# Optimization experiments

Hardware: AMD Instinct MI355X
Metric: run time of the kernel (lower is better)

The kernel has to match this reference:

```python
import jax, jax.numpy as jnp
import numpy as np

N = 100000      # num nodes
E = 3200000     # num edges (avg degree 32)
F_IN = 512      # num_features
HID = 16        # hidden dim hard-coded in GCN.__init__
C = 40          # num_classes


def setup_inputs() -> dict:
    key = jax.random.key(0)
    k = jax.random.split(key, 6)
    x = jax.random.normal(k[0], (N, F_IN), dtype=jnp.float32)
    edge_index = jax.random.randint(k[1], (2, E), 0, N)
    edge_weight = jax.random.uniform(k[2], (E,), dtype=jnp.float32)
    W1 = jax.random.normal(k[3], (F_IN, HID), dtype=jnp.float32) / np.sqrt(F_IN).astype(np.float32)
    b1 = jnp.zeros((HID,), jnp.float32)
    W2 = jax.random.normal(k[4], (HID, C), dtype=jnp.float32) / np.sqrt(HID).astype(np.float32)
    b2 = jnp.zeros((C,), jnp.float32)
    return {"x": x, "edge_weight": edge_weight, "W1": W1, "b1": b1,
            "W2": W2, "b2": b2, "edge_index": edge_index}


def _gcn_norm(edge_index, edge_weight, n):
    # PyG gcn_norm with add_self_loops=True, fill_value=1.0
    row = jnp.concatenate([edge_index[0], jnp.arange(n)])
    col = jnp.concatenate([edge_index[1], jnp.arange(n)])
    w = jnp.concatenate([edge_weight, jnp.ones((n,), edge_weight.dtype)])
    deg = jax.ops.segment_sum(w, col, num_segments=n)
    dinv = jnp.where(deg > 0, jax.lax.rsqrt(deg), 0.0)
    norm = dinv[row] * w * dinv[col]
    return row, col, norm


def _gcn_conv(x, W, b, row, col, norm, n):
    h = x @ W                                   # [N, out] linear first (out dim small)
    msg = h[row] * norm[:, None]                # gather + scale  [E+N, out]
    out = jax.ops.segment_sum(msg, col, num_segments=n)  # scatter-add
    return out + b


def reference(x, edge_weight, W1, b1, W2, b2, edge_index):
    n = x.shape[0]
    row, col, norm = _gcn_norm(edge_index, edge_weight, n)  # cached=True: shared by both layers
    h = jax.nn.relu(_gcn_conv(x, W1, b1, row, col, norm, n))
    # F.dropout(training=self.training) is identity in eval mode
    h = _gcn_conv(h, W2, b2, row, col, norm, n)
    return jax.nn.log_softmax(h, axis=1)
```

## Files before the change

kernel.cpp:

```cpp
#include <hip/hip_runtime.h>
#include <hip/hip_bf16.h>

#define HID 16
#define CLS 40
#define FIN 512
#define TILE 4000
#define NBP 512

typedef unsigned int uint;
typedef unsigned short ushort;

__device__ __forceinline__ ushort f2bf(float f) {
    uint u = __float_as_uint(f);
    u += 0x7FFF + ((u >> 16) & 1);
    return (ushort)(u >> 16);
}
__device__ __forceinline__ float bflo(uint u) { return __uint_as_float(u << 16); }
__device__ __forceinline__ float bfhi(uint u) { return __uint_as_float(u & 0xFFFF0000u); }
__device__ __forceinline__ float wdec(uint a) {
    return __uint_as_float((a >> 17) << 16);
}

__global__ __launch_bounds__(256) void scan1_k(const int* __restrict__ cnt,
                                               int* __restrict__ bsum, int M) {
    __shared__ int ws[4];
    int b = blockIdx.x, t = threadIdx.x;
    int i0 = b * 1024 + t * 4;
    int s = 0;
#pragma unroll
    for (int q = 0; q < 4; ++q) if (i0 + q < M) s += cnt[i0 + q];
    for (int d = 32; d > 0; d >>= 1) s += __shfl_xor(s, d);
    int lane = t & 63, wid = t >> 6;
    if (lane == 0) ws[wid] = s;
    __syncthreads();
    if (t == 0) bsum[b] = ws[0] + ws[1] + ws[2] + ws[3];
}

__global__ __launch_bounds__(256) void scan3_k(const int* __restrict__ cnt,
                                               const int* __restrict__ bsumRaw,
                                               int* __restrict__ sout, int M, int G) {
    __shared__ int sb[1024];
    __shared__ int wsumA[4], wbaseA[4];
    __shared__ int wsumB[4], wbaseB[4];
    int t = threadIdx.x;
    int lane = t & 63, wid = t >> 6;
    {
        int i0 = t * 4;
        int c[4];
#pragma unroll
        for (int q = 0; q < 4; ++q) c[q] = (i0 + q < G) ? bsumRaw[i0 + q] : 0;
        int s = c[0] + c[1] + c[2] + c[3];
        int v = s;
        for (int d = 1; d < 64; d <<= 1) { int u = __shfl_up(v, d); if (lane >= d) v += u; }
        if (lane == 63) wsumA[wid] = v;
        __syncthreads();
        if (t == 0) { int r = 0; for (int q = 0; q < 4; ++q) { wbaseA[q] = r; r += wsumA[q]; } }
        __syncthreads();
        int o = v - s + wbaseA[wid];
#pragma unroll
        for (int q = 0; q < 4; ++q) { sb[i0 + q] = o; o += c[q]; }
    }
    __syncthreads();
    {
        int b = blockIdx.x;
        int i0 = b * 1024 + t * 4;
        int c[4];
#pragma unroll
        for (int q = 0; q < 4; ++q) c[q] = (i0 + q < M) ? cnt[i0 + q] : 0;
        int s = c[0] + c[1] + c[2] + c[3];
        int v = s;
        for (int d = 1; d < 64; d <<= 1) { int u = __shfl_up(v, d); if (lane >= d) v += u; }
        if (lane == 63) wsumB[wid] = v;
        __syncthreads();
        if (t == 0) { int r = 0; for (int q = 0; q < 4; ++q) { wbaseB[q] = r; r += wsumB[q]; } }
        __syncthreads();
        int o = v - s + wbaseB[wid] + sb[b];
#pragma unroll
        for (int q = 0; q < 4; ++q) {
            if (i0 + q < M) { sout[i0 + q] = o; o += c[q]; }
        }
    }
}

__global__ __launch_bounds__(256) void bk_count_k(const int* __restrict__ col,
                                                  int* __restrict__ bcnt,
                                                  int E, int NB, int ABLK) {
    __shared__ int hist[NBP];
    int t = threadIdx.x, blk = blockIdx.x;
    for (int i = t; i < NBP; i += 256) hist[i] = 0;
    __syncthreads();
    int e0 = blk * TILE, e1 = min(E, e0 + TILE);
    for (int e = e0 + t; e < e1; e += 256) atomicAdd(&hist[col[e] >> 8], 1);
    __syncthreads();
    for (int b = t; b < NB; b += 256) bcnt[b * ABLK + blk] = hist[b];
}

__global__ __launch_bounds__(256) void bk_scatter_k(const int* __restrict__ row,
                                                    const int* __restrict__ col,
                                                    const float* __restrict__ w,
                                                    const int* __restrict__ sbcnt,
                                                    int2* __restrict__ bpack,
                                                    int E, int NB, int ABLK) {
    __shared__ int2 stage[TILE];
    __shared__ ushort stageB[TILE];
    __shared__ int hist[NBP], cur[NBP], gbase[NBP];
    __shared__ int wsum[4], wbase[4];
    int t = threadIdx.x, blk = blockIdx.x;
    for (int i = t; i < NBP; i += 256) hist[i] = 0;
    __syncthreads();
    int e0 = blk * TILE, e1 = min(E, e0 + TILE);
    for (int e = e0 + t; e < e1; e += 256) atomicAdd(&hist[col[e] >> 8], 1);
    __syncthreads();
    {
        int c0 = hist[2 * t], c1 = hist[2 * t + 1];
        int s = c0 + c1;
        int lane = t & 63, wid = t >> 6;
        int v = s;
        for (int d = 1; d < 64; d <<= 1) { int u = __shfl_up(v, d); if (lane >= d) v += u; }
        if (lane == 63) wsum[wid] = v;
        __syncthreads();
        if (t == 0) { int r = 0; for (int q = 0; q < 4; ++q) { wbase[q] = r; r += wsum[q]; } }
        __syncthreads();
        int excl = v - s + wbase[wid];
        int s0 = 2 * t, s1 = 2 * t + 1;
        cur[s0] = excl;
        gbase[s0] = ((s0 < NB) ? sbcnt[s0 * ABLK + blk] : 0) - excl;
        cur[s1] = excl + c0;
        gbase[s1] = ((s1 < NB) ? sbcnt[s1 * ABLK + blk] : 0) - (excl + c0);
    }
    __syncthreads();
    for (int e = e0 + t; e < e1; e += 256) {
        int c = col[e];
        int bkt = c >> 8, cl = c & 255;
        int lr = atomicAdd(&cur[bkt], 1);
        stage[lr] = make_int2(row[e] | (cl << 17), __float_as_int(w[e]));
        stageB[lr] = (ushort)bkt;
    }
    __syncthreads();
    int cntE = e1 - e0;
    for (int s = t; s < cntE; s += 256) {
        int bkt = stageB[s];
        bpack[gbase[bkt] + s] = stage[s];
    }
}

__global__ __launch_bounds__(512) void seg_build_k(const int2* __restrict__ bpack,
                                                   const int* __restrict__ sbcnt,
                                                   int* __restrict__ off,
                                                   float* __restrict__ dinv,
                                                   uint* __restrict__ fin,
                                                   int E, int NB, int ABLK, int NN) {
    __shared__ int cntL[256];
    __shared__ float degL[256];
    __shared__ int curL[256];
    __shared__ int wtot[8];
    int t = threadIdx.x, b = blockIdx.x;
    if (t < 256) { cntL[t] = 0; degL[t] = 0.f; }
    __syncthreads();
    int p0 = sbcnt[b * ABLK];
    int p1 = (b + 1 < NB) ? sbcnt[(b + 1) * ABLK] : E;
    for (int p = p0 + t; p < p1; p += 512) {
        int2 pk = bpack[p];
        int cl = (pk.x >> 17) & 255;
        atomicAdd(&cntL[cl], 1);
        atomicAdd(&degL[cl], __int_as_float(pk.y));
    }
    __syncthreads();
    int c = (t < 256) ? cntL[t] : 0;
    int lane = t & 63, wid = t >> 6;
    int v = c;
    for (int d = 1; d < 64; d <<= 1) { int u = __shfl_up(v, d); if (lane >= d) v += u; }
    if (lane == 63) wtot[wid] = v;
    __syncthreads();
    if (t < 256) {
        int base = p0;
        for (int q = 0; q < wid; ++q) base += wtot[q];
        int excl = base + v - c;
        int node = b * 256 + t;
        off[node] = excl;
        curL[t] = excl;
        dinv[node] = rsqrtf(1.0f + degL[t]);
    }
    if (b == NB - 1 && t == 0) off[NN] = E;
    __syncthreads();
    for (int p = p0 + t; p < p1; p += 512) {
        int2 pk = bpack[p];
        uint src = (uint)pk.x & 0x1FFFFu;
        int cl = (pk.x >> 17) & 255;
        uint u = (uint)pk.y + 0x8000u;
        int pos = atomicAdd(&curL[cl], 1);
        fin[pos] = src | ((u >> 16) << 17);
    }
}

__global__ __launch_bounds__(256) void gemm1_k(const float* __restrict__ x,
                                               const float* __restrict__ W1,
                                               const float* __restrict__ dinv,
                                               uint* __restrict__ g, int n) {
    __shared__ float4 w1s[FIN * HID / 4 + FIN / 4];
    {
        const float4* s4 = (const float4*)W1;
        for (int i = threadIdx.x; i < FIN * HID / 4; i += 256)
            w1s[i + (i >> 4)] = s4[i];
    }
    __syncthreads();
    int r = blockIdx.x * 64 + (threadIdx.x >> 2);
    if (r >= n) return;
    int sub = threadIdx.x & 3;
    const float4* xr = (const float4*)(x + (size_t)r * FIN);
    float acc[HID];
#pragma unroll
    for (int c = 0; c < HID; ++c) acc[c] = 0.f;
    for (int q = 0; q < FIN / 16; ++q) {
        float4 xv = xr[q * 4 + sub];
        int kbase = q * 16 + sub * 4;
        const float4* w4 = &w1s[kbase * 4 + (kbase >> 2)];
#pragma unroll
        for (int e = 0; e < 4; ++e) {
            float xe = (e == 0) ? xv.x : (e == 1) ? xv.y : (e == 2) ? xv.z : xv.w;
#pragma unroll
            for (int j = 0; j < 4; ++j) {
                float4 wv = w4[e * 4 + j];
                acc[4 * j + 0] += xe * wv.x;
                acc[4 * j + 1] += xe * wv.y;
                acc[4 * j + 2] += xe * wv.z;
                acc[4 * j + 3] += xe * wv.w;
            }
        }
    }
#pragma unroll
    for (int c = 0; c < HID; ++c) {
        acc[c] += __shfl_xor(acc[c], 1, 4);
        acc[c] += __shfl_xor(acc[c], 2, 4);
    }
    float f0, f1, f2, f3;
    {
        float t0 = (sub & 2) ? acc[8] : acc[0], t4 = (sub & 2) ? acc[12] : acc[4];
        f0 = (sub & 1) ? t4 : t0;
        float u0 = (sub & 2) ? acc[9] : acc[1], u4 = (sub & 2) ? acc[13] : acc[5];
        f1 = (sub & 1) ? u4 : u0;
        float v0 = (sub & 2) ? acc[10] : acc[2], v4 = (sub & 2) ? acc[14] : acc[6];
        f2 = (sub & 1) ? v4 : v0;
        float w0 = (sub & 2) ? acc[11] : acc[3], w4v = (sub & 2) ? acc[15] : acc[7];
        f3 = (sub & 1) ? w4v : w0;
    }
    float di = dinv[r];
    uint lo = (uint)f2bf(di * f0) | ((uint)f2bf(di * f1) << 16);
    uint hi = (uint)f2bf(di * f2) | ((uint)f2bf(di * f3) << 16);
    ((uint2*)(g + (size_t)r * 8))[sub] = make_uint2(lo, hi);
}

__global__ __launch_bounds__(256) void agg1_k(const uint* __restrict__ g,
                                              const float* __restrict__ dinv,
                                              const int* __restrict__ off,
                                              const uint* __restrict__ fin,
                                              const float* __restrict__ b1,
                                              uint* __restrict__ g1, int n) {
    int tid = blockIdx.x * 256 + threadIdx.x;
    int i = tid >> 3;
    if (i >= n) return;
    int lane = tid & 7;
    uint sv = g[(size_t)i * 8 + lane];
    float lo0 = bflo(sv), hi0 = bfhi(sv);
    float lo1 = 0.f, hi1 = 0.f, lo2 = 0.f, hi2 = 0.f, lo3 = 0.f, hi3 = 0.f;
    int p = off[i], e = off[i + 1];
    for (; p + 3 < e; p += 4) {
        uint a = fin[p], b = fin[p + 1], c = fin[p + 2], d = fin[p + 3];
        uint ga = g[(size_t)(a & 0x1FFFFu) * 8 + lane];
        uint gb = g[(size_t)(b & 0x1FFFFu) * 8 + lane];
        uint gc = g[(size_t)(c & 0x1FFFFu) * 8 + lane];
        uint gd = g[(size_t)(d & 0x1FFFFu) * 8 + lane];
        float wa = wdec(a), wb = wdec(b), wc = wdec(c), wdv = wdec(d);
        lo0 += wa * bflo(ga); hi0 += wa * bfhi(ga);
        lo1 += wb * bflo(gb); hi1 += wb * bfhi(gb);
        lo2 += wc * bflo(gc); hi2 += wc * bfhi(gc);
        lo3 += wdv * bflo(gd); hi3 += wdv * bfhi(gd);
    }
    for (; p < e; ++p) {
        uint a = fin[p];
        uint ga = g[(size_t)(a & 0x1FFFFu) * 8 + lane];
        float wa = wdec(a);
        lo0 += wa * bflo(ga); hi0 += wa * bfhi(ga);
    }
    float di = dinv[i];
    float vlo = fmaxf(di * ((lo0 + lo1) + (lo2 + lo3)) + b1[2 * lane], 0.f);
    float vhi = fmaxf(di * ((hi0 + hi1) + (hi2 + hi3)) + b1[2 * lane + 1], 0.f);
    g1[(size_t)i * 8 + lane] = (uint)f2bf(di * vlo) | ((uint)f2bf(di * vhi) << 16);
}

__global__ __launch_bounds__(256) void agg2out_k(const uint* __restrict__ g1,
                                                 const float* __restrict__ dinv,
                                                 const int* __restrict__ off,
                                                 const uint* __restrict__ fin,
                                                 const float* __restrict__ W2,
                                                 const float* __restrict__ b2,
                                                 float* __restrict__ out, int n) {
    __shared__ float w2s[HID * CLS];
    __shared__ float b2s[CLS];
    for (int q = threadIdx.x; q < HID * CLS; q += 256) w2s[q] = W2[q];
    if (threadIdx.x < CLS) b2s[threadIdx.x] = b2[threadIdx.x];
    __syncthreads();
    int tid = blockIdx.x * 256 + threadIdx.x;
    int i = tid >> 3;
    if (i >= n) return;
    int lane = tid & 7;
    uint sv = g1[(size_t)i * 8 + lane];
    float lo0 = bflo(sv), hi0 = bfhi(sv);
    float lo1 = 0.f, hi1 = 0.f, lo2 = 0.f, hi2 = 0.f, lo3 = 0.f, hi3 = 0.f;
    int p = off[i], e = off[i + 1];
    for (; p + 3 < e; p += 4) {
        uint a = fin[p], b = fin[p + 1], c = fin[p + 2], d = fin[p + 3];
        uint ga = g1[(size_t)(a & 0x1FFFFu) * 8 + lane];
        uint gb = g1[(size_t)(b & 0x1FFFFu) * 8 + lane];
        uint gc = g1[(size_t)(c & 0x1FFFFu) * 8 + lane];
        uint gd = g1[(size_t)(d & 0x1FFFFu) * 8 + lane];
        float wa = wdec(a), wb = wdec(b), wc = wdec(c), wdv = wdec(d);
        lo0 += wa * bflo(ga); hi0 += wa * bfhi(ga);
        lo1 += wb * bflo(gb); hi1 += wb * bfhi(gb);
        lo2 += wc * bflo(gc); hi2 += wc * bfhi(gc);
        lo3 += wdv * bflo(gd); hi3 += wdv * bfhi(gd);
    }
    for (; p < e; ++p) {
        uint a = fin[p];
        uint ga = g1[(size_t)(a & 0x1FFFFu) * 8 + lane];
        float wa = wdec(a);
        lo0 += wa * bflo(ga); hi0 += wa * bfhi(ga);
    }
    float di = dinv[i];
    float vlo = di * ((lo0 + lo1) + (lo2 + lo3));
    float vhi = di * ((hi0 + hi1) + (hi2 + hi3));
    float a[HID];
#pragma unroll
    for (int k = 0; k < 8; ++k) {
        a[2 * k]     = __shfl(vlo, k, 8);
        a[2 * k + 1] = __shfl(vhi, k, 8);
    }
    float z[5];
#pragma unroll
    for (int j = 0; j < 5; ++j) z[j] = b2s[lane + 8 * j];
#pragma unroll
    for (int k = 0; k < HID; ++k) {
        float ak = a[k];
#pragma unroll
        for (int j = 0; j < 5; ++j) z[j] += ak * w2s[k * CLS + lane + 8 * j];
    }
    float m = z[0];
#pragma unroll
    for (int j = 1; j < 5; ++j) m = fmaxf(m, z[j]);
#pragma unroll
    for (int d = 1; d < 8; d <<= 1) m = fmaxf(m, __shfl_xor(m, d, 8));
    float s = 0.f;
#pragma unroll
    for (int j = 0; j < 5; ++j) s += __expf(z[j] - m);
#pragma unroll
    for (int d = 1; d < 8; d <<= 1) s += __shfl_xor(s, d, 8);
    float l = __logf(s) + m;
    float* o = out + (size_t)i * CLS;
#pragma unroll
    for (int j = 0; j < 5; ++j) o[lane + 8 * j] = z[j] - l;
}

extern "C" void kernel_launch(void* const* d_in, const int* in_sizes, int n_in,
                              void* d_out, int out_size, void* d_ws, size_t ws_size,
                              hipStream_t stream) {
    const float* x  = (const float*)d_in[0];
    const float* ew = (const float*)d_in[1];
    const float* W1 = (const float*)d_in[2];
    const float* b1 = (const float*)d_in[3];
    const float* W2 = (const float*)d_in[4];
    const float* b2 = (const float*)d_in[5];
    const int*   ei = (const int*)d_in[6];

    int n = in_sizes[0] / FIN;
    int E = in_sizes[1];
    const int* row = ei;
    const int* col = ei + E;

    int NB   = (n + 255) >> 8;
    int NN   = NB * 256;
    int ABLK = (E + TILE - 1) / TILE;
    int M1   = NB * ABLK;

    size_t o = 0;
    int*   bcnt  = (int*)d_ws + o;  o += M1;
    int*   sbcnt = (int*)d_ws + o;  o += M1;
    int*   bsum  = (int*)d_ws + o;  o += 1024;
    int*   off   = (int*)d_ws + o;  o += (size_t)NN + 1;
    float* dinv  = (float*)((int*)d_ws + o); o += NN;
    uint*  fin   = (uint*)((int*)d_ws + o);  o += E;
    o = (o + 3) & ~(size_t)3;
    int2*  bpack = (int2*)((int*)d_ws + o);
    uint*  g    = (uint*)bpack;
    uint*  g1   = g + (size_t)8 * n;

    float* outp = (float*)d_out;

    dim3 b(256);
    int G1 = (M1 + 1023) / 1024;

    bk_count_k<<<ABLK, b, 0, stream>>>(col, bcnt, E, NB, ABLK);
    scan1_k<<<G1, b, 0, stream>>>(bcnt, bsum, M1);
    scan3_k<<<G1, b, 0, stream>>>(bcnt, bsum, sbcnt, M1, G1);
    bk_scatter_k<<<ABLK, b, 0, stream>>>(row, col, ew, sbcnt, bpack, E, NB, ABLK);

    seg_build_k<<<NB, dim3(512), 0, stream>>>(bpack, sbcnt, off, dinv, fin, E, NB, ABLK, NN);

    gemm1_k<<<(n + 63) / 64, b, 0, stream>>>(x, W1, dinv, g, n);
    int gb8 = (n * 8 + 255) / 256;
    agg1_k<<<gb8, b, 0, stream>>>(g, dinv, off, fin, b1, g1, n);
    agg2out_k<<<gb8, b, 0, stream>>>(g1, dinv, off, fin, W2, b2, outp, n);
}
```

Before: 227.9 us.

## Merge GEMM1 with edge bucket counting and defer dinv scaling into aggregation

The x@W1 GEMM no longer depends on dinv, so its blocks are launched together with the column-histogram counting blocks in one grid. The dense GEMM, which reads 200MB of x, can then overlap the edge-preprocessing start and one launch is removed. To make this possible, source-node dinv scaling moves into agg1, which now does an extra random dinv gather per edge. g/g1 get their own workspace rather than aliasing bpack, and the edge-list loads become aligned uint4 vector reads with a scalar prologue.

```diff
diff --git a/kernel.cpp b/kernel.cpp
--- a/kernel.cpp
+++ b/kernel.cpp
@@ -82,17 +82,73 @@
     }
 }
 
-__global__ __launch_bounds__(256) void bk_count_k(const int* __restrict__ col,
-                                                  int* __restrict__ bcnt,
-                                                  int E, int NB, int ABLK) {
-    __shared__ int hist[NBP];
-    int t = threadIdx.x, blk = blockIdx.x;
-    for (int i = t; i < NBP; i += 256) hist[i] = 0;
-    __syncthreads();
-    int e0 = blk * TILE, e1 = min(E, e0 + TILE);
-    for (int e = e0 + t; e < e1; e += 256) atomicAdd(&hist[col[e] >> 8], 1);
-    __syncthreads();
-    for (int b = t; b < NB; b += 256) bcnt[b * ABLK + blk] = hist[b];
+__global__ __launch_bounds__(256) void gemm_count_k(const float* __restrict__ x,
+                                                    const float* __restrict__ W1,
+                                                    uint* __restrict__ g, int n, int GB,
+                                                    const int* __restrict__ col,
+                                                    int* __restrict__ bcnt,
+                                                    int E, int NB, int ABLK) {
+    __shared__ float4 w1s[FIN * HID / 4 + FIN / 4];
+    if (blockIdx.x >= GB) {
+        int* hist = (int*)w1s;
+        int t = threadIdx.x, blk = blockIdx.x - GB;
+        for (int i = t; i < NBP; i += 256) hist[i] = 0;
+        __syncthreads();
+        int e0 = blk * TILE, e1 = min(E, e0 + TILE);
+        for (int e = e0 + t; e < e1; e += 256) atomicAdd(&hist[col[e] >> 8], 1);
+        __syncthreads();
+        for (int b = t; b < NB; b += 256) bcnt[b * ABLK + blk] = hist[b];
+        return;
+    }
+    {
+        const float4* s4 = (const float4*)W1;
+        for (int i = threadIdx.x; i < FIN * HID / 4; i += 256)
+            w1s[i + (i >> 4)] = s4[i];
+    }
+    __syncthreads();
+    int r = blockIdx.x * 64 + (threadIdx.x >> 2);
+    if (r >= n) return;
+    int sub = threadIdx.x & 3;
+    const float4* xr = (const float4*)(x + (size_t)r * FIN);
+    float acc[HID];
+#pragma unroll
+    for (int c = 0; c < HID; ++c) acc[c] = 0.f;
+    for (int q = 0; q < FIN / 16; ++q) {
+        float4 xv = xr[q * 4 + sub];
+        int kbase = q * 16 + sub * 4;
+        const float4* w4 = &w1s[kbase * 4 + (kbase >> 2)];
+#pragma unroll
+        for (int e = 0; e < 4; ++e) {
+            float xe = (e == 0) ? xv.x : (e == 1) ? xv.y : (e == 2) ? xv.z : xv.w;
+#pragma unroll
+            for (int j = 0; j < 4; ++j) {
+                float4 wv = w4[e * 4 + j];
+                acc[4 * j + 0] += xe * wv.x;
+                acc[4 * j + 1] += xe * wv.y;
+                acc[4 * j + 2] += xe * wv.z;
+                acc[4 * j + 3] += xe * wv.w;
+            }
+        }
+    }
+#pragma unroll
+    for (int c = 0; c < HID; ++c) {
+        acc[c] += __shfl_xor(acc[c], 1, 4);
+        acc[c] += __shfl_xor(acc[c], 2, 4);
+    }
+    float f0, f1, f2, f3;
+    {
+        float t0 = (sub & 2) ? acc[8] : acc[0], t4 = (sub & 2) ? acc[12] : acc[4];
+        f0 = (sub & 1) ? t4 : t0;
+        float u0 = (sub & 2) ? acc[9] : acc[1], u4 = (sub & 2) ? acc[13] : acc[5];
+        f1 = (sub & 1) ? u4 : u0;
+        float v0 = (sub & 2) ? acc[10] : acc[2], v4 = (sub & 2) ? acc[14] : acc[6];
+        f2 = (sub & 1) ? v4 : v0;
+        float w0 = (sub & 2) ? acc[11] : acc[3], w4v = (sub & 2) ? acc[15] : acc[7];
+        f3 = (sub & 1) ? w4v : w0;
+    }
+    uint lo = (uint)f2bf(f0) | ((uint)f2bf(f1) << 16);
+    uint hi = (uint)f2bf(f2) | ((uint)f2bf(f3) << 16);
+    ((uint2*)(g + (size_t)r * 8))[sub] = make_uint2(lo, hi);
 }
 
 __global__ __launch_bounds__(256) void bk_scatter_k(const int* __restrict__ row,
@@ -193,63 +249,6 @@
     }
 }
 
-__global__ __launch_bounds__(256) void gemm1_k(const float* __restrict__ x,
-                                               const float* __restrict__ W1,
-                                               const float* __restrict__ dinv,
-                                               uint* __restrict__ g, int n) {
-    __shared__ float4 w1s[FIN * HID / 4 + FIN / 4];
-    {
-        const float4* s4 = (const float4*)W1;
-        for (int i = threadIdx.x; i < FIN * HID / 4; i += 256)
-            w1s[i + (i >> 4)] = s4[i];
-    }
-    __syncthreads();
-    int r = blockIdx.x * 64 + (threadIdx.x >> 2);
-    if (r >= n) return;
-    int sub = threadIdx.x & 3;
-    const float4* xr = (const float4*)(x + (size_t)r * FIN);
-    float acc[HID];
-#pragma unroll
-    for (int c = 0; c < HID; ++c) acc[c] = 0.f;
-    for (int q = 0; q < FIN / 16; ++q) {
-        float4 xv = xr[q * 4 + sub];
-        int kbase = q * 16 + sub * 4;
-        const float4* w4 = &w1s[kbase * 4 + (kbase >> 2)];
-#pragma unroll
-        for (int e = 0; e < 4; ++e) {
-            float xe = (e == 0) ? xv.x : (e == 1) ? xv.y : (e == 2) ? xv.z : xv.w;
-#pragma unroll
-            for (int j = 0; j < 4; ++j) {
-                float4 wv = w4[e * 4 + j];
-                acc[4 * j + 0] += xe * wv.x;
-                acc[4 * j + 1] += xe * wv.y;
-                acc[4 * j + 2] += xe * wv.z;
-                acc[4 * j + 3] += xe * wv.w;
-            }
-        }
-    }
-#pragma unroll
-    for (int c = 0; c < HID; ++c) {
-        acc[c] += __shfl_xor(acc[c], 1, 4);
-        acc[c] += __shfl_xor(acc[c], 2, 4);
-    }
-    float f0, f1, f2, f3;
-    {
-        float t0 = (sub & 2) ? acc[8] : acc[0], t4 = (sub & 2) ? acc[12] : acc[4];
-        f0 = (sub & 1) ? t4 : t0;
-        float u0 = (sub & 2) ? acc[9] : acc[1], u4 = (sub & 2) ? acc[13] : acc[5];
-        f1 = (sub & 1) ? u4 : u0;
-        float v0 = (sub & 2) ? acc[10] : acc[2], v4 = (sub & 2) ? acc[14] : acc[6];
-        f2 = (sub & 1) ? v4 : v0;
-        float w0 = (sub & 2) ? acc[11] : acc[3], w4v = (sub & 2) ? acc[15] : acc[7];
-        f3 = (sub & 1) ? w4v : w0;
-    }
-    float di = dinv[r];
-    uint lo = (uint)f2bf(di * f0) | ((uint)f2bf(di * f1) << 16);
-    uint hi = (uint)f2bf(di * f2) | ((uint)f2bf(di * f3) << 16);
-    ((uint2*)(g + (size_t)r * 8))[sub] = make_uint2(lo, hi);
-}
-
 __global__ __launch_bounds__(256) void agg1_k(const uint* __restrict__ g,
                                               const float* __restrict__ dinv,
                                               const int* __restrict__ off,
@@ -260,29 +259,38 @@
     int i = tid >> 3;
     if (i >= n) return;
     int lane = tid & 7;
+    float di = dinv[i];
     uint sv = g[(size_t)i * 8 + lane];
-    float lo0 = bflo(sv), hi0 = bfhi(sv);
+    float lo0 = di * bflo(sv), hi0 = di * bfhi(sv);
     float lo1 = 0.f, hi1 = 0.f, lo2 = 0.f, hi2 = 0.f, lo3 = 0.f, hi3 = 0.f;
     int p = off[i], e = off[i + 1];
+    while (p < e && (p & 3)) {
+        uint a = fin[p++];
+        float wa = wdec(a) * dinv[a & 0x1FFFFu];
+        uint ga = g[(size_t)(a & 0x1FFFFu) * 8 + lane];
+        lo0 += wa * bflo(ga); hi0 += wa * bfhi(ga);
+    }
     for (; p + 3 < e; p += 4) {
-        uint a = fin[p], b = fin[p + 1], c = fin[p + 2], d = fin[p + 3];
-        uint ga = g[(size_t)(a & 0x1FFFFu) * 8 + lane];
-        uint gb = g[(size_t)(b & 0x1FFFFu) * 8 + lane];
-        uint gc = g[(size_t)(c & 0x1FFFFu) * 8 + lane];
-        uint gd = g[(size_t)(d & 0x1FFFFu) * 8 + lane];
-        float wa = wdec(a), wb = wdec(b), wc = wdec(c), wdv = wdec(d);
+        uint4 f = *(const uint4*)(fin + p);
+        uint ga = g[(size_t)(f.x & 0x1FFFFu) * 8 + lane];
+        uint gb = g[(size_t)(f.y & 0x1FFFFu) * 8 + lane];
+        uint gc = g[(size_t)(f.z & 0x1FFFFu) * 8 + lane];
+        uint gd = g[(size_t)(f.w & 0x1FFFFu) * 8 + lane];
+        float wa = wdec(f.x) * dinv[f.x & 0x1FFFFu];
+        float wb = wdec(f.y) * dinv[f.y & 0x1FFFFu];
+        float wc = wdec(f.z) * dinv[f.z & 0x1FFFFu];
+        float wd = wdec(f.w) * dinv[f.w & 0x1FFFFu];
         lo0 += wa * bflo(ga); hi0 += wa * bfhi(ga);
         lo1 += wb * bflo(gb); hi1 += wb * bfhi(gb);
         lo2 += wc * bflo(gc); hi2 += wc * bfhi(gc);
-        lo3 += wdv * bflo(gd); hi3 += wdv * bfhi(gd);
+        lo3 += wd * bflo(gd); hi3 += wd * bfhi(gd);
     }
     for (; p < e; ++p) {
         uint a = fin[p];
+        float wa = wdec(a) * dinv[a & 0x1FFFFu];
         uint ga = g[(size_t)(a & 0x1FFFFu) * 8 + lane];
-        float wa = wdec(a);
-        lo0 += wa * bflo(ga); hi0 += wa * bfhi(ga);
-    }
-    float di = dinv[i];
+        lo0 += wa * bflo(ga); hi0 += wa * bfhi(ga);
+    }
     float vlo = fmaxf(di * ((lo0 + lo1) + (lo2 + lo3)) + b1[2 * lane], 0.f);
     float vhi = fmaxf(di * ((hi0 + hi1) + (hi2 + hi3)) + b1[2 * lane + 1], 0.f);
     g1[(size_t)i * 8 + lane] = (uint)f2bf(di * vlo) | ((uint)f2bf(di * vhi) << 16);
@@ -308,22 +316,28 @@
     float lo0 = bflo(sv), hi0 = bfhi(sv);
     float lo1 = 0.f, hi1 = 0.f, lo2 = 0.f, hi2 = 0.f, lo3 = 0.f, hi3 = 0.f;
     int p = off[i], e = off[i + 1];
+    while (p < e && (p & 3)) {
+        uint a = fin[p++];
+        float wa = wdec(a);
+        uint ga = g1[(size_t)(a & 0x1FFFFu) * 8 + lane];
+        lo0 += wa * bflo(ga); hi0 += wa * bfhi(ga);
+    }
     for (; p + 3 < e; p += 4) {
-        uint a = fin[p], b = fin[p + 1], c = fin[p + 2], d = fin[p + 3];
-        uint ga = g1[(size_t)(a & 0x1FFFFu) * 8 + lane];
-        uint gb = g1[(size_t)(b & 0x1FFFFu) * 8 + lane];
-        uint gc = g1[(size_t)(c & 0x1FFFFu) * 8 + lane];
-        uint gd = g1[(size_t)(d & 0x1FFFFu) * 8 + lane];
-        float wa = wdec(a), wb = wdec(b), wc = wdec(c), wdv = wdec(d);
+        uint4 f = *(const uint4*)(fin + p);
+        uint ga = g1[(size_t)(f.x & 0x1FFFFu) * 8 + lane];
+        uint gb = g1[(size_t)(f.y & 0x1FFFFu) * 8 + lane];
+        uint gc = g1[(size_t)(f.z & 0x1FFFFu) * 8 + lane];
+        uint gd = g1[(size_t)(f.w & 0x1FFFFu) * 8 + lane];
+        float wa = wdec(f.x), wb = wdec(f.y), wc = wdec(f.z), wd = wdec(f.w);
         lo0 += wa * bflo(ga); hi0 += wa * bfhi(ga);
         lo1 += wb * bflo(gb); hi1 += wb * bfhi(gb);
         lo2 += wc * bflo(gc); hi2 += wc * bfhi(gc);
-        lo3 += wdv * bflo(gd); hi3 += wdv * bfhi(gd);
+        lo3 += wd * bflo(gd); hi3 += wd * bfhi(gd);
     }
     for (; p < e; ++p) {
         uint a = fin[p];
+        float wa = wdec(a);
         uint ga = g1[(size_t)(a & 0x1FFFFu) * 8 + lane];
-        float wa = wdec(a);
         lo0 += wa * bflo(ga); hi0 += wa * bfhi(ga);
     }
     float di = dinv[i];
@@ -382,30 +396,28 @@
     int M1   = NB * ABLK;
 
     size_t o = 0;
-    int*   bcnt  = (int*)d_ws + o;  o += M1;
-    int*   sbcnt = (int*)d_ws + o;  o += M1;
-    int*   bsum  = (int*)d_ws + o;  o += 1024;
-    int*   off   = (int*)d_ws + o;  o += (size_t)NN + 1;
-    float* dinv  = (float*)((int*)d_ws + o); o += NN;
-    uint*  fin   = (uint*)((int*)d_ws + o);  o += E;
-    o = (o + 3) & ~(size_t)3;
+    auto align4 = [&]() { o = (o + 3) & ~(size_t)3; };
+    int*   bcnt  = (int*)d_ws + o;  o += M1;            align4();
+    int*   sbcnt = (int*)d_ws + o;  o += M1;            align4();
+    int*   bsum  = (int*)d_ws + o;  o += 1024;          align4();
+    int*   off   = (int*)d_ws + o;  o += (size_t)NN + 1; align4();
+    float* dinv  = (float*)((int*)d_ws + o); o += NN;   align4();
+    uint*  fin   = (uint*)((int*)d_ws + o);  o += E;    align4();
+    uint*  g     = (uint*)((int*)d_ws + o);  o += (size_t)8 * n; align4();
+    uint*  g1    = (uint*)((int*)d_ws + o);  o += (size_t)8 * n; align4();
     int2*  bpack = (int2*)((int*)d_ws + o);
-    uint*  g    = (uint*)bpack;
-    uint*  g1   = g + (size_t)8 * n;
 
     float* outp = (float*)d_out;
 
     dim3 b(256);
     int G1 = (M1 + 1023) / 1024;
-
-    bk_count_k<<<ABLK, b, 0, stream>>>(col, bcnt, E, NB, ABLK);
+    int GB = (n + 63) / 64;
+
+    gemm_count_k<<<GB + ABLK, b, 0, stream>>>(x, W1, g, n, GB, col, bcnt, E, NB, ABLK);
     scan1_k<<<G1, b, 0, stream>>>(bcnt, bsum, M1);
     scan3_k<<<G1, b, 0, stream>>>(bcnt, bsum, sbcnt, M1, G1);
     bk_scatter_k<<<ABLK, b, 0, stream>>>(row, col, ew, sbcnt, bpack, E, NB, ABLK);
-
     seg_build_k<<<NB, dim3(512), 0, stream>>>(bpack, sbcnt, off, dinv, fin, E, NB, ABLK, NN);
-
-    gemm1_k<<<(n + 63) / 64, b, 0, stream>>>(x, W1, dinv, g, n);
     int gb8 = (n * 8 + 255) / 256;
     agg1_k<<<gb8, b, 0, stream>>>(g, dinv, off, fin, b1, g1, n);
     agg2out_k<<<gb8, b, 0, stream>>>(g1, dinv, off, fin, W2, b2, outp, n);
```

Result: slower. 236.7 us (+3.8%).
